# Kernel tuning notes

Measured on AMD Instinct MI355X. Metric: run time of the kernel, lower is better.

The kernel has to match this reference:

```python
import jax, jax.numpy as jnp
import numpy as np

B = 2
C = 1024
H = 16
D = C // H  # 64
L_S, L_T, L_C = 2048, 1024, 512
MODS = ["shape", "texture", "color"]
SCALE_RMS = np.sqrt(D).astype(np.float32)
SCALE_ATTN = 1.0 / np.sqrt(D).astype(np.float32)


def _rms(x, gamma):
    # F.normalize(x, dim=-1) * gamma * sqrt(dim); x: [B,L,H,D], gamma: [H,D]
    n = jnp.linalg.norm(x, axis=-1, keepdims=True)
    return x / jnp.maximum(n, 1e-12) * gamma * SCALE_RMS


def _sdpa(q, k, v):
    # q: [B,Lq,H,D], k/v: [B,Lk,H,D] -> [B,Lq,H,D]
    s = jnp.einsum("blhd,bmhd->bhlm", q, k) * SCALE_ATTN
    a = jax.nn.softmax(s, axis=-1)
    return jnp.einsum("bhlm,bmhd->blhd", a, v)


def setup_inputs() -> dict:
    key = jax.random.key(0)
    ks = jax.random.split(key, 32)
    inp = {}
    lens = {"shape": L_S, "texture": L_T, "color": L_C}
    i = 0
    for m in MODS:
        inp[f"x_{m}"] = jax.random.normal(ks[i], (B, lens[m], C), jnp.float32); i += 1
        inp[f"Wqkv_{m}"] = jax.random.normal(ks[i], (C, 3 * C), jnp.float32) * 0.02; i += 1
        inp[f"bqkv_{m}"] = jnp.zeros((3 * C,), jnp.float32)
        inp[f"gq_{m}"] = jnp.ones((H, D), jnp.float32)
        inp[f"gk_{m}"] = jnp.ones((H, D), jnp.float32)
        inp[f"Wout_{m}"] = jax.random.normal(ks[i], (C, C), jnp.float32) * 0.02; i += 1
        inp[f"bout_{m}"] = jnp.zeros((C,), jnp.float32)
    return inp


def _forward(x_shape, x_texture, x_color,
             Wqkv_shape, bqkv_shape, gq_shape, gk_shape, Wout_shape, bout_shape,
             Wqkv_texture, bqkv_texture, gq_texture, gk_texture, Wout_texture, bout_texture,
             Wqkv_color, bqkv_color, gq_color, gk_color, Wout_color, bout_color):
    xs = {"shape": x_shape, "texture": x_texture, "color": x_color}
    Wqkv = {"shape": Wqkv_shape, "texture": Wqkv_texture, "color": Wqkv_color}
    bqkv = {"shape": bqkv_shape, "texture": bqkv_texture, "color": bqkv_color}
    gq = {"shape": gq_shape, "texture": gq_texture, "color": gq_color}
    gk = {"shape": gk_shape, "texture": gk_texture, "color": gk_color}
    Wout = {"shape": Wout_shape, "texture": Wout_texture, "color": Wout_color}
    bout = {"shape": bout_shape, "texture": bout_texture, "color": bout_color}

    q, k, v = {}, {}, {}
    for m in MODS:
        L = xs[m].shape[1]
        qkv = (xs[m] @ Wqkv[m] + bqkv[m]).reshape(B, L, 3, H, D)
        _q, _k, _v = qkv[:, :, 0], qkv[:, :, 1], qkv[:, :, 2]
        q[m] = _rms(_q, gq[m])
        k[m] = _rms(_k, gk[m])
        v[m] = _v

    # protected modality attends only to itself
    h = {"shape": _sdpa(q["shape"], k["shape"], v["shape"])}

    # other modalities: joint attention over [others ; detached protected]
    others = ["texture", "color"]
    q_o = jnp.concatenate([q[m] for m in others], axis=1)
    k_all = jnp.concatenate([k[m] for m in others] + [jax.lax.stop_gradient(k["shape"])], axis=1)
    v_all = jnp.concatenate([v[m] for m in others] + [jax.lax.stop_gradient(v["shape"])], axis=1)
    h_o = _sdpa(q_o, k_all, v_all)
    h["texture"] = h_o[:, :L_T]
    h["color"] = h_o[:, L_T:L_T + L_C]

    outs = []
    for m in MODS:
        L = h[m].shape[1]
        outs.append(h[m].reshape(B, L, C) @ Wout[m] + bout[m])
    return tuple(outs)


def reference(x_shape, x_texture, x_color,
              Wqkv_shape, bqkv_shape, gq_shape, gk_shape, Wout_shape, bout_shape,
              Wqkv_texture, bqkv_texture, gq_texture, gk_texture, Wout_texture, bout_texture,
              Wqkv_color, bqkv_color, gq_color, gk_color, Wout_color, bout_color):
    return _forward(x_shape, x_texture, x_color,
                    Wqkv_shape, bqkv_shape, gq_shape, gk_shape, Wout_shape, bout_shape,
                    Wqkv_texture, bqkv_texture, gq_texture, gk_texture, Wout_texture, bout_texture,
                    Wqkv_color, bqkv_color, gq_color, gk_color, Wout_color, bout_color)
```

## Files before the change

### kernel.cpp

```cpp
#include <hip/hip_runtime.h>
#include <hip/hip_bf16.h>
#include <stdint.h>

typedef unsigned short u16;
typedef __attribute__((ext_vector_type(8))) short bf16x8;
typedef __attribute__((ext_vector_type(4))) float f32x4;
typedef __attribute__((ext_vector_type(4))) unsigned short u16x4;
typedef __attribute__((ext_vector_type(8))) unsigned short u16x8;

#define DEV __device__ __forceinline__

DEV u16 f2bf(float f){
  unsigned u = __float_as_uint(f);
  return (u16)((u + 0x7FFFu + ((u >> 16) & 1u)) >> 16);
}
DEV float b2f(u16 v){ return __uint_as_float(((unsigned)v) << 16); }

DEV f32x4 MFMA(bf16x8 a, bf16x8 b, f32x4 c){
  return __builtin_amdgcn_mfma_f32_16x16x32_bf16(a, b, c, 0, 0, 0);
}

__global__ __launch_bounds__(256) void cvt_f32_bf16(const float* __restrict__ in,
                                                    u16* __restrict__ out, int n4){
  int i = blockIdx.x * 256 + threadIdx.x;
  if (i >= n4) return;
  f32x4 v = ((const f32x4*)in)[i];
  u16x4 o;
  o[0] = f2bf(v[0]); o[1] = f2bf(v[1]); o[2] = f2bf(v[2]); o[3] = f2bf(v[3]);
  ((u16x4*)out)[i] = o;
}

__global__ __launch_bounds__(256) void tcvt(const float* __restrict__ in, u16* __restrict__ out,
                                            int R, int C){
  __shared__ float tile[64][65];
  int c0 = blockIdx.x * 64, r0 = blockIdx.y * 64;
  int t = threadIdx.x;
#pragma unroll
  for (int j = 0; j < 16; j++){
    int idx = j * 256 + t;
    int r = idx >> 6, c = idx & 63;
    tile[r][c] = in[(size_t)(r0 + r) * C + c0 + c];
  }
  __syncthreads();
#pragma unroll
  for (int j = 0; j < 16; j++){
    int idx = j * 256 + t;
    int c = idx >> 6, r = idx & 63;
    out[(size_t)(c0 + c) * R + r0 + r] = f2bf(tile[r][c]);
  }
}

template<int F32OUT>
__global__ __launch_bounds__(256) void gemm_bt(const u16* __restrict__ A, const u16* __restrict__ Bt,
                                               const float* __restrict__ bias, void* __restrict__ outp,
                                               int M, int N, int K){
  __shared__ __align__(16) u16 smA[128 * 40];
  __shared__ __align__(16) u16 smB[128 * 40];
  int t = threadIdx.x;
  int lane = t & 63, w = t >> 6;
  int wr = w >> 1, wc = w & 1;
  int li = lane & 15, g = lane >> 4;
  int m0 = blockIdx.y * 128, n0 = blockIdx.x * 128;

  int srow = t >> 2, sseg = (t & 3) * 8;
  const u16* Ap0 = A  + (size_t)(m0 + srow) * K + sseg;
  const u16* Ap1 = Ap0 + (size_t)64 * K;
  const u16* Bp0 = Bt + (size_t)(n0 + srow) * K + sseg;
  const u16* Bp1 = Bp0 + (size_t)64 * K;

  f32x4 acc[4][4] = {};
  u16x8 a0 = *(const u16x8*)Ap0, a1 = *(const u16x8*)Ap1;
  u16x8 b0 = *(const u16x8*)Bp0, b1 = *(const u16x8*)Bp1;

  for (int kt = 32; kt <= K; kt += 32){
    __syncthreads();
    *(u16x8*)&smA[srow * 40 + sseg]        = a0;
    *(u16x8*)&smA[(64 + srow) * 40 + sseg] = a1;
    *(u16x8*)&smB[srow * 40 + sseg]        = b0;
    *(u16x8*)&smB[(64 + srow) * 40 + sseg] = b1;
    __syncthreads();
    if (kt < K){
      a0 = *(const u16x8*)(Ap0 + kt); a1 = *(const u16x8*)(Ap1 + kt);
      b0 = *(const u16x8*)(Bp0 + kt); b1 = *(const u16x8*)(Bp1 + kt);
    }
    bf16x8 af[4], bfr[4];
#pragma unroll
    for (int mf = 0; mf < 4; mf++)
      af[mf] = *(const bf16x8*)&smA[(wr * 64 + mf * 16 + li) * 40 + g * 8];
#pragma unroll
    for (int nf = 0; nf < 4; nf++)
      bfr[nf] = *(const bf16x8*)&smB[(wc * 64 + nf * 16 + li) * 40 + g * 8];
#pragma unroll
    for (int mf = 0; mf < 4; mf++)
#pragma unroll
      for (int nf = 0; nf < 4; nf++)
        acc[mf][nf] = MFMA(af[mf], bfr[nf], acc[mf][nf]);
  }

#pragma unroll
  for (int mf = 0; mf < 4; mf++){
    int row = m0 + wr * 64 + mf * 16 + g * 4;
#pragma unroll
    for (int nf = 0; nf < 4; nf++){
      int col = n0 + wc * 64 + nf * 16 + li;
      float bs = bias[col];
#pragma unroll
      for (int r = 0; r < 4; r++){
        float v = acc[mf][nf][r] + bs;
        if (F32OUT) ((float*)outp)[(size_t)(row + r) * N + col] = v;
        else        ((u16*)outp)[(size_t)(row + r) * N + col]  = f2bf(v);
      }
    }
  }
}

__global__ __launch_bounds__(256) void rms_scatter(const u16* __restrict__ qkvb, int L,
                                                   const float* __restrict__ gq, const float* __restrict__ gk,
                                                   u16* __restrict__ qdst, int qL, int qoff,
                                                   u16* __restrict__ kdst, int kvoff){
  int tok = blockIdx.x;
  int b = tok / L, l = tok - b * L;
  int t = threadIdx.x;
  int c = t * 4;
  int h = t >> 4;
  int d = c & 63;
  const u16* rowq = qkvb + (size_t)tok * 3072 + c;
  u16x4 qv = *(const u16x4*)rowq;
  u16x4 kv = *(const u16x4*)(rowq + 1024);
  float qf[4], kf[4], ssq = 0.f, ssk = 0.f;
#pragma unroll
  for (int j = 0; j < 4; j++){
    qf[j] = b2f(qv[j]); kf[j] = b2f(kv[j]);
    ssq += qf[j] * qf[j]; ssk += kf[j] * kf[j];
  }
#pragma unroll
  for (int msk = 1; msk < 16; msk <<= 1){
    ssq += __shfl_xor(ssq, msk);
    ssk += __shfl_xor(ssk, msk);
  }
  float sq = 8.0f / fmaxf(sqrtf(ssq), 1e-12f);
  float sk = 8.0f / fmaxf(sqrtf(ssk), 1e-12f);
  u16x4 qo, ko;
#pragma unroll
  for (int j = 0; j < 4; j++){
    qo[j] = f2bf(qf[j] * sq * gq[h * 64 + d + j]);
    ko[j] = f2bf(kf[j] * sk * gk[h * 64 + d + j]);
  }
  *(u16x4*)(qdst + ((size_t)(b * 16 + h) * qL + qoff + l) * 64 + d) = qo;
  *(u16x4*)(kdst + ((size_t)(b * 16 + h) * 3584 + kvoff + l) * 64 + d) = ko;
}

__global__ __launch_bounds__(256) void vtrans(const u16* __restrict__ qkvb, int L,
                                              u16* __restrict__ vT, int kvoff){
  __shared__ u16 tile[64][65];
  int l0 = blockIdx.x * 64; int h = blockIdx.y; int b = blockIdx.z;
  int t = threadIdx.x;
#pragma unroll
  for (int j = 0; j < 16; j++){
    int idx = j * 256 + t;
    int r = idx >> 6, d = idx & 63;
    tile[r][d] = qkvb[(size_t)(b * L + l0 + r) * 3072 + 2048 + h * 64 + d];
  }
  __syncthreads();
#pragma unroll
  for (int j = 0; j < 16; j++){
    int idx = j * 256 + t;
    int d = idx >> 6, r = idx & 63;
    vT[((size_t)(b * 16 + h) * 64 + d) * 3584 + kvoff + l0 + r] = tile[r][d];
  }
}

__global__ __launch_bounds__(128, 3) void attn(const u16* __restrict__ q0, const u16* __restrict__ q1,
                                               const u16* __restrict__ kmat, const u16* __restrict__ vTm,
                                               u16* __restrict__ ob0, u16* __restrict__ ob1,
                                               u16* __restrict__ ob2){
  __shared__ __align__(16) u16 smK[64 * 72];
  __shared__ __align__(16) u16 smV[64 * 72];
  __shared__ __align__(16) u16 smP[2][32 * 68];
  int lin = blockIdx.x;
  bool t1 = lin < 768;
  int rel = t1 ? lin : lin - 768;
  int qb = rel >> 5, hb = rel & 31;
  int h = hb & 15, b = hb >> 4;
  int bh = b * 16 + h;
  const u16* qp = t1 ? q1 : q0;
  int Lq  = t1 ? 1536 : 2048;
  int kvo = t1 ? 0    : 1536;
  int Lk  = t1 ? 3584 : 2048;
  u16* out0 = t1 ? ob1 : ob0;  int L0 = t1 ? 1024 : 2048;
  u16* out1 = t1 ? ob2 : ob0;  int L1 = t1 ? 512  : 2048;

  int t = threadIdx.x, lane = t & 63, w = t >> 6;
  int li = lane & 15, g = lane >> 4;

  const u16* qbase = qp + ((size_t)bh * Lq + qb * 64 + w * 32) * 64;
  bf16x8 qa[2][2];
#pragma unroll
  for (int qg = 0; qg < 2; qg++)
#pragma unroll
    for (int kh = 0; kh < 2; kh++)
      qa[qg][kh] = *(const bf16x8*)(qbase + (size_t)(qg * 16 + li) * 64 + kh * 32 + g * 8);

  f32x4 acc[2][4] = {};
  float mrunL[2] = {-3.0e38f, -3.0e38f};
  float lsumL[2] = {0.f, 0.f};

  const u16* kbase = kmat + ((size_t)bh * 3584 + kvo) * 64;
  const u16* vbase = vTm + (size_t)bh * 64 * 3584 + kvo;
  u16* pp = &smP[w][0];

  const float SC = 0.125f * 1.44269504088896340736f;

  u16x8 ka[4], va[4];
#pragma unroll
  for (int j = 0; j < 4; j++){
    int u = t + j * 128; int ur = u >> 3, us = (u & 7) * 8;
    ka[j] = *(const u16x8*)(kbase + (size_t)ur * 64 + us);
    va[j] = *(const u16x8*)(vbase + (size_t)ur * 3584 + us);
  }

  for (int kt = 0; kt < Lk; kt += 64){
    __syncthreads();
#pragma unroll
    for (int j = 0; j < 4; j++){
      int u = t + j * 128; int ur = u >> 3, us = (u & 7) * 8;
      *(u16x8*)&smK[ur * 72 + us] = ka[j];
      *(u16x8*)&smV[ur * 72 + us] = va[j];
    }
    __syncthreads();
    if (kt + 64 < Lk){
#pragma unroll
      for (int j = 0; j < 4; j++){
        int u = t + j * 128; int ur = u >> 3, us = (u & 7) * 8;
        ka[j] = *(const u16x8*)(kbase + (size_t)(kt + 64 + ur) * 64 + us);
        va[j] = *(const u16x8*)(vbase + (size_t)ur * 3584 + kt + 64 + us);
      }
    }

    f32x4 sT[2][4];
#pragma unroll
    for (int kg = 0; kg < 4; kg++){
      bf16x8 kf0 = *(const bf16x8*)&smK[(kg * 16 + li) * 72 + g * 8];
      bf16x8 kf1 = *(const bf16x8*)&smK[(kg * 16 + li) * 72 + 32 + g * 8];
#pragma unroll
      for (int qg = 0; qg < 2; qg++){
        f32x4 z = {};
        z = MFMA(kf0, qa[qg][0], z);
        sT[qg][kg] = MFMA(kf1, qa[qg][1], z);
      }
    }

#pragma unroll
    for (int qg = 0; qg < 2; qg++){
      float sc[16];
#pragma unroll
      for (int kg = 0; kg < 4; kg++)
#pragma unroll
        for (int r = 0; r < 4; r++) sc[kg * 4 + r] = sT[qg][kg][r] * SC;
      float m01 = fmaxf(fmaxf(sc[0], sc[1]),   fmaxf(sc[2], sc[3]));
      float m23 = fmaxf(fmaxf(sc[4], sc[5]),   fmaxf(sc[6], sc[7]));
      float m45 = fmaxf(fmaxf(sc[8], sc[9]),   fmaxf(sc[10], sc[11]));
      float m67 = fmaxf(fmaxf(sc[12], sc[13]), fmaxf(sc[14], sc[15]));
      float rm = fmaxf(fmaxf(m01, m23), fmaxf(m45, m67));
      rm = fmaxf(rm, __shfl_xor(rm, 16));
      rm = fmaxf(rm, __shfl_xor(rm, 32));
      float mo = mrunL[qg];
      float mn = fmaxf(mo, rm);
      float al = __builtin_exp2f(mo - mn);
      mrunL[qg] = mn;
      float ps = 0.f;
      u16x4 pk[4];
#pragma unroll
      for (int kg = 0; kg < 4; kg++){
#pragma unroll
        for (int r = 0; r < 4; r++){
          float p = __builtin_exp2f(sc[kg * 4 + r] - mn);
          ps += p;
          pk[kg][r] = f2bf(p);
        }
      }
      lsumL[qg] = lsumL[qg] * al + ps;
#pragma unroll
      for (int dt = 0; dt < 4; dt++)
#pragma unroll
        for (int r = 0; r < 4; r++) acc[qg][dt][r] *= al;
#pragma unroll
      for (int kg = 0; kg < 4; kg++)
        *(u16x4*)&pp[(qg * 16 + li) * 68 + kg * 16 + g * 4] = pk[kg];
    }

    bf16x8 pf[2][2];
#pragma unroll
    for (int qg = 0; qg < 2; qg++){
      pf[qg][0] = *(const bf16x8*)&pp[(qg * 16 + li) * 68 + g * 8];
      pf[qg][1] = *(const bf16x8*)&pp[(qg * 16 + li) * 68 + 32 + g * 8];
    }
#pragma unroll
    for (int dt = 0; dt < 4; dt++){
      bf16x8 vf0 = *(const bf16x8*)&smV[(dt * 16 + li) * 72 + g * 8];
      bf16x8 vf1 = *(const bf16x8*)&smV[(dt * 16 + li) * 72 + 32 + g * 8];
#pragma unroll
      for (int qg = 0; qg < 2; qg++){
        acc[qg][dt] = MFMA(vf0, pf[qg][0], acc[qg][dt]);
        acc[qg][dt] = MFMA(vf1, pf[qg][1], acc[qg][dt]);
      }
    }
  }

#pragma unroll
  for (int qg = 0; qg < 2; qg++){
    float ls = lsumL[qg];
    ls += __shfl_xor(ls, 16);
    ls += __shfl_xor(ls, 32);
    float inv = 1.0f / ls;
    int qi = qb * 64 + w * 32 + qg * 16 + li;
    u16* dst; size_t basei;
    if (qi < L0){ dst = out0; basei = ((size_t)(b * L0 + qi)) * 1024 + h * 64; }
    else        { dst = out1; basei = ((size_t)(b * L1 + (qi - L0))) * 1024 + h * 64; }
#pragma unroll
    for (int dt = 0; dt < 4; dt++){
      u16x4 o;
#pragma unroll
      for (int r = 0; r < 4; r++) o[r] = f2bf(acc[qg][dt][r] * inv);
      *(u16x4*)&dst[basei + dt * 16 + g * 4] = o;
    }
  }
}

extern "C" void kernel_launch(void* const* d_in, const int* in_sizes, int n_in,
                              void* d_out, int out_size, void* d_ws, size_t ws_size,
                              hipStream_t stream){
  (void)in_sizes; (void)n_in; (void)out_size; (void)ws_size;
  const float* x[3]    = {(const float*)d_in[0],  (const float*)d_in[7],  (const float*)d_in[14]};
  const float* Wqkv[3] = {(const float*)d_in[1],  (const float*)d_in[8],  (const float*)d_in[15]};
  const float* bqkv[3] = {(const float*)d_in[2],  (const float*)d_in[9],  (const float*)d_in[16]};
  const float* gq[3]   = {(const float*)d_in[3],  (const float*)d_in[10], (const float*)d_in[17]};
  const float* gk[3]   = {(const float*)d_in[4],  (const float*)d_in[11], (const float*)d_in[18]};
  const float* Wout[3] = {(const float*)d_in[5],  (const float*)d_in[12], (const float*)d_in[19]};
  const float* bout[3] = {(const float*)d_in[6],  (const float*)d_in[13], (const float*)d_in[20]};
  float* outp = (float*)d_out;

  const int Ms[3] = {4096, 2048, 1024};
  const int Ls[3] = {2048, 1024, 512};
  const int kvoffs[3] = {1536, 0, 1024};

  u16* base = (u16*)d_ws;
  size_t off = 0;
  auto nxt = [&](size_t e){ u16* r = base + off; off += e; return r; };
  u16* xbf[3];  for (int m = 0; m < 3; m++) xbf[m]  = nxt((size_t)Ms[m] * 1024);
  u16* WqT[3];  for (int m = 0; m < 3; m++) WqT[m]  = nxt((size_t)3072 * 1024);
  u16* WoT[3];  for (int m = 0; m < 3; m++) WoT[m]  = nxt((size_t)1024 * 1024);
  u16* qkvb[3]; for (int m = 0; m < 3; m++) qkvb[m] = nxt((size_t)Ms[m] * 3072);
  u16* qA = nxt((size_t)2 * 16 * 2048 * 64);
  u16* qB = nxt((size_t)2 * 16 * 1536 * 64);
  u16* kB = nxt((size_t)2 * 16 * 3584 * 64);
  u16* vT = WqT[0];
  u16* hb[3]; for (int m = 0; m < 3; m++) hb[m] = xbf[m];

  for (int m = 0; m < 3; m++){
    int n4 = Ms[m] * 1024 / 4;
    cvt_f32_bf16<<<n4 / 256, 256, 0, stream>>>(x[m], xbf[m], n4);
    tcvt<<<dim3(3072 / 64, 1024 / 64), 256, 0, stream>>>(Wqkv[m], WqT[m], 1024, 3072);
    tcvt<<<dim3(1024 / 64, 1024 / 64), 256, 0, stream>>>(Wout[m], WoT[m], 1024, 1024);
  }
  for (int m = 0; m < 3; m++)
    gemm_bt<0><<<dim3(3072 / 128, Ms[m] / 128), 256, 0, stream>>>(
        xbf[m], WqT[m], bqkv[m], qkvb[m], Ms[m], 3072, 1024);
  rms_scatter<<<Ms[0], 256, 0, stream>>>(qkvb[0], Ls[0], gq[0], gk[0], qA, 2048, 0,    kB, 1536);
  rms_scatter<<<Ms[1], 256, 0, stream>>>(qkvb[1], Ls[1], gq[1], gk[1], qB, 1536, 0,    kB, 0);
  rms_scatter<<<Ms[2], 256, 0, stream>>>(qkvb[2], Ls[2], gq[2], gk[2], qB, 1536, 1024, kB, 1024);
  for (int m = 0; m < 3; m++)
    vtrans<<<dim3(Ls[m] / 64, 16, 2), 256, 0, stream>>>(qkvb[m], Ls[m], vT, kvoffs[m]);
  attn<<<1792, 128, 0, stream>>>(qA, qB, kB, vT, hb[0], hb[1], hb[2]);
  float* outs[3] = {outp, outp + (size_t)4096 * 1024, outp + (size_t)6144 * 1024};
  for (int m = 0; m < 3; m++)
    gemm_bt<1><<<dim3(1024 / 128, Ms[m] / 128), 256, 0, stream>>>(
        hb[m], WoT[m], bout[m], outs[m], Ms[m], 1024, 1024);
}
```

Measured before the change: 563.9 us.

## Fold softmax scale into q norm, skip redundant rescale, pack bf16 converts

The attention scale and log2(e) factor move into the q normalization kernel, which removes a per-score multiply in the flash-attention inner loop. The running-max rescale of the accumulators is now skipped when no lane's row max increased. Probabilities are packed to bf16 with the hardware v_cvt_pk_bf16_f32 instruction instead of manual rounding. s_setprio is raised around the MFMA blocks to favour matrix issue across waves. Storing q with the extra scale changes its bf16 rounding slightly, and the inline asm depends on that instruction being available on this target.

```diff
diff --git a/kernel.cpp b/kernel.cpp
--- a/kernel.cpp
+++ b/kernel.cpp
@@ -3,8 +3,10 @@
 #include <stdint.h>
 
 typedef unsigned short u16;
+typedef unsigned int u32;
 typedef __attribute__((ext_vector_type(8))) short bf16x8;
 typedef __attribute__((ext_vector_type(4))) float f32x4;
+typedef __attribute__((ext_vector_type(2))) unsigned int u32x2;
 typedef __attribute__((ext_vector_type(4))) unsigned short u16x4;
 typedef __attribute__((ext_vector_type(8))) unsigned short u16x8;
 
@@ -15,6 +17,12 @@
   return (u16)((u + 0x7FFFu + ((u >> 16) & 1u)) >> 16);
 }
 DEV float b2f(u16 v){ return __uint_as_float(((unsigned)v) << 16); }
+
+DEV u32 cvtpk(float lo, float hi){
+  u32 r;
+  asm("v_cvt_pk_bf16_f32 %0, %1, %2" : "=v"(r) : "v"(lo), "v"(hi));
+  return r;
+}
 
 DEV f32x4 MFMA(bf16x8 a, bf16x8 b, f32x4 c){
   return __builtin_amdgcn_mfma_f32_16x16x32_bf16(a, b, c, 0, 0, 0);
@@ -138,7 +146,7 @@
     ssq += __shfl_xor(ssq, msk);
     ssk += __shfl_xor(ssk, msk);
   }
-  float sq = 8.0f / fmaxf(sqrtf(ssq), 1e-12f);
+  float sq = 1.44269504088896340736f / fmaxf(sqrtf(ssq), 1e-12f);
   float sk = 8.0f / fmaxf(sqrtf(ssk), 1e-12f);
   u16x4 qo, ko;
 #pragma unroll
@@ -209,8 +217,6 @@
   const u16* vbase = vTm + (size_t)bh * 64 * 3584 + kvo;
   u16* pp = &smP[w][0];
 
-  const float SC = 0.125f * 1.44269504088896340736f;
-
   u16x8 ka[4], va[4];
 #pragma unroll
   for (int j = 0; j < 4; j++){
@@ -238,6 +244,7 @@
     }
 
     f32x4 sT[2][4];
+    __builtin_amdgcn_s_setprio(1);
 #pragma unroll
     for (int kg = 0; kg < 4; kg++){
       bf16x8 kf0 = *(const bf16x8*)&smK[(kg * 16 + li) * 72 + g * 8];
@@ -249,44 +256,51 @@
         sT[qg][kg] = MFMA(kf1, qa[qg][1], z);
       }
     }
-
+    __builtin_amdgcn_s_setprio(0);
+
+    float rm[2];
 #pragma unroll
     for (int qg = 0; qg < 2; qg++){
-      float sc[16];
-#pragma unroll
-      for (int kg = 0; kg < 4; kg++)
-#pragma unroll
-        for (int r = 0; r < 4; r++) sc[kg * 4 + r] = sT[qg][kg][r] * SC;
-      float m01 = fmaxf(fmaxf(sc[0], sc[1]),   fmaxf(sc[2], sc[3]));
-      float m23 = fmaxf(fmaxf(sc[4], sc[5]),   fmaxf(sc[6], sc[7]));
-      float m45 = fmaxf(fmaxf(sc[8], sc[9]),   fmaxf(sc[10], sc[11]));
-      float m67 = fmaxf(fmaxf(sc[12], sc[13]), fmaxf(sc[14], sc[15]));
-      float rm = fmaxf(fmaxf(m01, m23), fmaxf(m45, m67));
-      rm = fmaxf(rm, __shfl_xor(rm, 16));
-      rm = fmaxf(rm, __shfl_xor(rm, 32));
-      float mo = mrunL[qg];
-      float mn = fmaxf(mo, rm);
-      float al = __builtin_exp2f(mo - mn);
-      mrunL[qg] = mn;
+      float m01 = fmaxf(fmaxf(sT[qg][0][0], sT[qg][0][1]), fmaxf(sT[qg][0][2], sT[qg][0][3]));
+      float m23 = fmaxf(fmaxf(sT[qg][1][0], sT[qg][1][1]), fmaxf(sT[qg][1][2], sT[qg][1][3]));
+      float m45 = fmaxf(fmaxf(sT[qg][2][0], sT[qg][2][1]), fmaxf(sT[qg][2][2], sT[qg][2][3]));
+      float m67 = fmaxf(fmaxf(sT[qg][3][0], sT[qg][3][1]), fmaxf(sT[qg][3][2], sT[qg][3][3]));
+      float v = fmaxf(fmaxf(m01, m23), fmaxf(m45, m67));
+      v = fmaxf(v, __shfl_xor(v, 16));
+      v = fmaxf(v, __shfl_xor(v, 32));
+      rm[qg] = v;
+    }
+
+    if (__any((rm[0] > mrunL[0]) | (rm[1] > mrunL[1]))){
+#pragma unroll
+      for (int qg = 0; qg < 2; qg++){
+        float mo = mrunL[qg];
+        float mn = fmaxf(mo, rm[qg]);
+        float al = __builtin_exp2f(mo - mn);
+        mrunL[qg] = mn;
+        lsumL[qg] *= al;
+#pragma unroll
+        for (int dt = 0; dt < 4; dt++)
+#pragma unroll
+          for (int r = 0; r < 4; r++) acc[qg][dt][r] *= al;
+      }
+    }
+
+#pragma unroll
+    for (int qg = 0; qg < 2; qg++){
+      float mn = mrunL[qg];
       float ps = 0.f;
-      u16x4 pk[4];
 #pragma unroll
       for (int kg = 0; kg < 4; kg++){
-#pragma unroll
-        for (int r = 0; r < 4; r++){
-          float p = __builtin_exp2f(sc[kg * 4 + r] - mn);
-          ps += p;
-          pk[kg][r] = f2bf(p);
-        }
-      }
-      lsumL[qg] = lsumL[qg] * al + ps;
-#pragma unroll
-      for (int dt = 0; dt < 4; dt++)
-#pragma unroll
-        for (int r = 0; r < 4; r++) acc[qg][dt][r] *= al;
-#pragma unroll
-      for (int kg = 0; kg < 4; kg++)
-        *(u16x4*)&pp[(qg * 16 + li) * 68 + kg * 16 + g * 4] = pk[kg];
+        float p0 = __builtin_exp2f(sT[qg][kg][0] - mn);
+        float p1 = __builtin_exp2f(sT[qg][kg][1] - mn);
+        float p2 = __builtin_exp2f(sT[qg][kg][2] - mn);
+        float p3 = __builtin_exp2f(sT[qg][kg][3] - mn);
+        ps += (p0 + p1) + (p2 + p3);
+        u32x2 pk; pk[0] = cvtpk(p0, p1); pk[1] = cvtpk(p2, p3);
+        *(u32x2*)&pp[(qg * 16 + li) * 68 + kg * 16 + g * 4] = pk;
+      }
+      lsumL[qg] += ps;
     }
 
     bf16x8 pf[2][2];
@@ -295,6 +309,7 @@
       pf[qg][0] = *(const bf16x8*)&pp[(qg * 16 + li) * 68 + g * 8];
       pf[qg][1] = *(const bf16x8*)&pp[(qg * 16 + li) * 68 + 32 + g * 8];
     }
+    __builtin_amdgcn_s_setprio(1);
 #pragma unroll
     for (int dt = 0; dt < 4; dt++){
       bf16x8 vf0 = *(const bf16x8*)&smV[(dt * 16 + li) * 72 + g * 8];
@@ -305,6 +320,7 @@
         acc[qg][dt] = MFMA(vf1, pf[qg][1], acc[qg][dt]);
       }
     }
+    __builtin_amdgcn_s_setprio(0);
   }
 
 #pragma unroll
```

New measurement: 542.4 us. 1.04x faster.
